# Optimization experiments

Hardware: AMD Instinct MI355X
Metric: run time of the kernel (lower is better)

The kernel has to match this reference:

```python
import jax, jax.numpy as jnp
import numpy as np
import math

B, S, IN_DIM = 2048, 60, 211
D, H, L, DFF, NC = 192, 6, 3, 768, 35
DK = D // H


def make_pe(seq_len, d_model):
    pos = np.arange(seq_len)[:, None].astype(np.float32)
    div = np.exp(np.arange(0, d_model, 2).astype(np.float32) * (-math.log(10000.0) / d_model))
    pe = np.zeros((seq_len, d_model), dtype=np.float32)
    pe[:, 0::2] = np.sin(pos * div)
    pe[:, 1::2] = np.cos(pos * div)
    return jnp.asarray(pe)


def setup_inputs() -> dict:
    key = jax.random.key(0)
    ks = jax.random.split(key, 24)
    r = lambda k, shape, fan: jax.random.normal(k, shape, jnp.float32) * (1.0 / np.sqrt(fan))
    inp = {
        'x': jax.random.normal(ks[0], (B, S, IN_DIM), jnp.float32),
        'W_in': r(ks[1], (IN_DIM, D), IN_DIM), 'b_in': jnp.zeros((D,), jnp.float32),
        'pe': make_pe(S, D),
        'Wq': r(ks[2], (L, D, D), D), 'bq': jnp.zeros((L, D), jnp.float32),
        'Wk': r(ks[3], (L, D, D), D), 'bk': jnp.zeros((L, D), jnp.float32),
        'Wv': r(ks[4], (L, D, D), D), 'bv': jnp.zeros((L, D), jnp.float32),
        'Wo': r(ks[5], (L, D, D), D), 'bo': jnp.zeros((L, D), jnp.float32),
        'W1': r(ks[6], (L, D, DFF), D), 'b1': jnp.zeros((L, DFF), jnp.float32),
        'W2': r(ks[7], (L, DFF, D), DFF), 'b2': jnp.zeros((L, D), jnp.float32),
        'g1': jnp.ones((L, D), jnp.float32), 'be1': jnp.zeros((L, D), jnp.float32),
        'g2': jnp.ones((L, D), jnp.float32), 'be2': jnp.zeros((L, D), jnp.float32),
        'Wc1': r(ks[8], (D, D // 2), D), 'bc1': jnp.zeros((D // 2,), jnp.float32),
        'Wc2': r(ks[9], (D // 2, NC), D // 2), 'bc2': jnp.zeros((NC,), jnp.float32),
    }
    return inp


def layer_norm(x, g, b, eps=1e-5):
    mu = jnp.mean(x, axis=-1, keepdims=True)
    var = jnp.mean((x - mu) ** 2, axis=-1, keepdims=True)
    return (x - mu) * jax.lax.rsqrt(var + eps) * g + b


def mha(x, Wq, bq, Wk, bk, Wv, bv, Wo, bo):
    Bs, Ss, _ = x.shape
    q = (x @ Wq + bq).reshape(Bs, Ss, H, DK)
    k = (x @ Wk + bk).reshape(Bs, Ss, H, DK)
    v = (x @ Wv + bv).reshape(Bs, Ss, H, DK)
    scores = jnp.einsum('bqhd,bkhd->bhqk', q, k) / jnp.sqrt(jnp.float32(DK))
    attn = jax.nn.softmax(scores, axis=-1)
    ctx = jnp.einsum('bhqk,bkhd->bqhd', attn, v).reshape(Bs, Ss, D)
    return ctx @ Wo + bo


def encoder_layer(x, Wq, bq, Wk, bk, Wv, bv, Wo, bo, W1, b1, W2, b2, g1, be1, g2, be2):
    attn_out = mha(x, Wq, bq, Wk, bk, Wv, bv, Wo, bo)
    x = layer_norm(x + attn_out, g1, be1)
    ff = jax.nn.gelu(x @ W1 + b1, approximate=False) @ W2 + b2
    return layer_norm(x + ff, g2, be2)


def reference(x, W_in, b_in, pe, Wq, bq, Wk, bk, Wv, bv, Wo, bo,
              W1, b1, W2, b2, g1, be1, g2, be2, Wc1, bc1, Wc2, bc2):
    h = x @ W_in + b_in + pe  # [B,S,D]
    for l in range(L):
        h = encoder_layer(h, Wq[l], bq[l], Wk[l], bk[l], Wv[l], bv[l], Wo[l], bo[l],
                          W1[l], b1[l], W2[l], b2[l], g1[l], be1[l], g2[l], be2[l])
    hidden = jax.nn.gelu(h @ Wc1 + bc1, approximate=False)
    return hidden @ Wc2 + bc2  # [B,S,NC]
```

## Files before the change

### kernel.cpp

```cpp
#include <hip/hip_runtime.h>
#include <cmath>

#define B_   2048
#define S_   60
#define NTOK (B_*S_)
#define IND_ 211
#define D_   192
#define H_   6
#define DK_  32
#define L_   3
#define DFF_ 768
#define NC_  35
#define DH_  96

typedef unsigned short us_t;
typedef us_t us8 __attribute__((ext_vector_type(8)));
typedef us_t us4 __attribute__((ext_vector_type(4)));
typedef short sh8 __attribute__((ext_vector_type(8)));
typedef float f4 __attribute__((ext_vector_type(4)));

#define MFMA(a, b, cc) __builtin_amdgcn_mfma_f32_16x16x32_bf16((a), (b), (cc), 0, 0, 0)
#define ZACC(A, M, N) \
    for (int _i = 0; _i < (M); ++_i) \
        for (int _j = 0; _j < (N); ++_j) { \
            A[_i][_j][0] = 0.f; A[_i][_j][1] = 0.f; A[_i][_j][2] = 0.f; A[_i][_j][3] = 0.f; }
#define ZACC1(A, N) \
    for (int _j = 0; _j < (N); ++_j) { \
        A[_j][0] = 0.f; A[_j][1] = 0.f; A[_j][2] = 0.f; A[_j][3] = 0.f; }

__device__ __forceinline__ float bf2f(us_t u) {
    union { unsigned int i; float f; } v; v.i = ((unsigned int)u) << 16; return v.f;
}
__device__ __forceinline__ us_t f2bf(float f) {
    union { float f; unsigned int i; } v; v.f = f;
    unsigned int r = v.i + 0x7fffu + ((v.i >> 16) & 1u);
    return (us_t)(r >> 16);
}
__device__ __forceinline__ float gelu_f(float v) {
    float u = v * (0.7978845608f + 0.0356774081f * v * v);
    float e = __expf(2.f * u);
    float t = 1.f - 2.f / (e + 1.f);
    return 0.5f * v * (1.f + t);
}
__device__ __forceinline__ void gld16(const us_t* g, us_t* s) {
    __builtin_amdgcn_global_load_lds(
        (const __attribute__((address_space(1))) unsigned int*)(g),
        (__attribute__((address_space(3))) unsigned int*)(s), 16, 0, 0);
}

__global__ void prep_misc(const float* __restrict__ W_in, const float* __restrict__ Wc1,
                          us_t* __restrict__ Wint, us_t* __restrict__ Wc1t)
{
    int e = blockIdx.x * 256 + threadIdx.x;
    const int n1 = 192 * 224, n2 = 96 * 192;
    if (e < n1) {
        int n = e / 224, kp = e % 224;
        Wint[e] = (kp < IND_) ? f2bf(W_in[(size_t)kp * D_ + n]) : (us_t)0;
    } else if (e < n1 + n2) {
        int r = e - n1;
        int n = r / 192, kp = r % 192;
        Wc1t[r] = f2bf(Wc1[(size_t)kp * DH_ + n]);
    }
}

__global__ void prep_qkvw(const float* __restrict__ Wq, const float* __restrict__ Wk,
                          const float* __restrict__ Wv, const float* __restrict__ Wo,
                          us_t* __restrict__ WI)
{
    int e = blockIdx.x * 256 + threadIdx.x;
    if (e >= L_ * 12 * 13824) return;
    int l = e / (12 * 13824), r = e % (12 * 13824);
    int t = r / 13824, q = r % 13824;
    int rw = q / 72, kk = q % 72;
    us_t v = 0;
    if (kk < 64) {
        int mat = (t < 9) ? (t / 3) : 3;
        int pc  = (t < 9) ? (t % 3) : (t - 9);
        const float* W = (mat == 0) ? Wq : (mat == 1) ? Wk : (mat == 2) ? Wv : Wo;
        v = f2bf(W[(size_t)l * 36864 + (size_t)(pc * 64 + kk) * D_ + rw]);
    }
    WI[e] = v;
}

__global__ void prep_ff(const float* __restrict__ W1, const float* __restrict__ W2,
                        us_t* __restrict__ W1T, us_t* __restrict__ W2T)
{
    int e = blockIdx.x * 256 + threadIdx.x;
    if (e >= L_ * 12 * 13824) return;
    int l = e / (12 * 13824), r = e % (12 * 13824);
    int tile = r / 13824, q = r % 13824;
    int col = q / 72, kk = q % 72;
    int cb = tile / 3, pc = tile % 3;
    us_t v1 = 0, v2 = 0;
    if (kk < 64) {
        v1 = f2bf(W1[((size_t)l * D_ + pc * 64 + kk) * DFF_ + cb * D_ + col]);
        v2 = f2bf(W2[((size_t)l * DFF_ + cb * D_ + pc * 64 + kk) * D_ + col]);
    }
    W1T[e] = v1; W2T[e] = v2;
}

__global__ __launch_bounds__(256) void inp_mfma(
    const float* __restrict__ x, const us_t* __restrict__ Wint,
    const float* __restrict__ b_in, const float* __restrict__ pe,
    us_t* __restrict__ h)
{
    __shared__ __align__(16) char smem[29696 + 27648];
    us_t* Xs = (us_t*)smem;
    us_t* Ws = (us_t*)(smem + 29696);
    const int tid = threadIdx.x;
    const int lane = tid & 63, wid = tid >> 6;
    const int g = lane >> 4, c = lane & 15;
    const int wr = wid >> 1, wc = wid & 1;
    const int row0 = blockIdx.x * 64;

    for (int e = tid; e < 64 * 224; e += 256) {
        int tok = e / 224, kp = e % 224;
        float v = (kp < IND_) ? x[(size_t)(row0 + tok) * IND_ + kp] : 0.f;
        Xs[tok * 232 + kp] = f2bf(v);
    }

    f4 acc[2][6];
    ZACC(acc, 2, 6);
    for (int pc = 0; pc < 4; ++pc) {
        __syncthreads();
        const int nk = (pc < 3) ? 64 : 32;
        const int per = nk / 8;
        for (int e = tid; e < 192 * per; e += 256) {
            int rw = e / per, v = e % per;
            *(us8*)&Ws[rw * 72 + v * 8] =
                *(const us8*)&Wint[(size_t)rw * 224 + pc * 64 + v * 8];
        }
        __syncthreads();
        for (int kk = 0; kk < nk / 32; ++kk) {
            const int ka = pc * 64 + kk * 32 + g * 8;
            const int kw = kk * 32 + g * 8;
            sh8 a0 = *(const sh8*)&Xs[(32 * wr + c) * 232 + ka];
            sh8 a1 = *(const sh8*)&Xs[(32 * wr + 16 + c) * 232 + ka];
            #pragma unroll
            for (int ni = 0; ni < 6; ++ni) {
                sh8 bf = *(const sh8*)&Ws[(96 * wc + 16 * ni + c) * 72 + kw];
                acc[0][ni] = MFMA(a0, bf, acc[0][ni]);
                acc[1][ni] = MFMA(a1, bf, acc[1][ni]);
            }
        }
    }
    #pragma unroll
    for (int ni = 0; ni < 6; ++ni) {
        const int col = 96 * wc + 16 * ni + c;
        const float bv = b_in[col];
        #pragma unroll
        for (int mi = 0; mi < 2; ++mi)
            #pragma unroll
            for (int r = 0; r < 4; ++r) {
                int tokg = row0 + 32 * wr + 16 * mi + 4 * g + r;
                int s = tokg % S_;
                float val = acc[mi][ni][r] + bv + pe[(size_t)s * D_ + col];
                h[(size_t)tokg * D_ + col] = f2bf(val);
            }
    }
}

__global__ __launch_bounds__(1024) void qkv_attn_wo(
    us_t* __restrict__ h, const us_t* __restrict__ WI,
    const float* __restrict__ bq, const float* __restrict__ bk,
    const float* __restrict__ bv, const float* __restrict__ bo,
    const float* __restrict__ g1, const float* __restrict__ be1)
{
    __shared__ __align__(16) char smem[159744];
    us_t* Xs  = (us_t*)smem;
    us_t* Qs  = (us_t*)(smem + 25600);
    us_t* Ks  = (us_t*)(smem + 51200);
    us_t* Vt  = (us_t*)(smem + 76800);
    us_t* Wsb = (us_t*)(smem + 104448);
    us_t* P6  = (us_t*)(smem + 104448);
    us_t* Cx  = (us_t*)(smem + 25600);
    float* eL = (float*)(smem + 51200);

    const int tid = threadIdx.x;
    const int lane = tid & 63, wid = tid >> 6;
    const int g = lane >> 4, c = lane & 15;
    const int wr = wid >> 2, wc = wid & 3;
    us_t* hb = h + (size_t)blockIdx.x * (S_ * D_);

    auto stageI = [&](int t) {
        const us_t* src = WI + (size_t)t * 13824;
        us_t* dst = Wsb + (size_t)(t & 1) * 13824;
        for (int i = wid; i < 27; i += 16)
            gld16(src + i * 512 + lane * 8, dst + i * 512);
    };

    for (int e = tid; e < 1536; e += 1024) {
        int tok = e / 24, v = e % 24;
        us8 u = {0, 0, 0, 0, 0, 0, 0, 0};
        if (tok < S_) u = *(const us8*)&hb[(size_t)tok * D_ + v * 8];
        *(us8*)&Xs[tok * 200 + v * 8] = u;
    }
    stageI(0);
    __syncthreads();

    for (int m = 0; m < 3; ++m) {
        const float* bb = (m == 0) ? bq : (m == 1) ? bk : bv;
        f4 acc[3];
        ZACC1(acc, 3);
        for (int pc = 0; pc < 3; ++pc) {
            const int t = m * 3 + pc;
            if (t < 8) stageI(t + 1);
            const us_t* W = Wsb + (size_t)(t & 1) * 13824;
            #pragma unroll
            for (int kk = 0; kk < 2; ++kk) {
                const int ka = pc * 64 + kk * 32 + g * 8;
                const int kw = kk * 32 + g * 8;
                sh8 a0 = *(const sh8*)&Xs[(16 * wr + c) * 200 + ka];
                #pragma unroll
                for (int ni = 0; ni < 3; ++ni) {
                    sh8 bf = *(const sh8*)&W[(48 * wc + 16 * ni + c) * 72 + kw];
                    acc[ni] = MFMA(a0, bf, acc[ni]);
                }
            }
            __syncthreads();
        }
        #pragma unroll
        for (int ni = 0; ni < 3; ++ni) {
            const int col = 48 * wc + 16 * ni + c;
            const float bval = bb[col];
            #pragma unroll
            for (int r = 0; r < 4; ++r) {
                int tok = 16 * wr + 4 * g + r;
                us_t o = f2bf(acc[ni][r] + bval);
                if (m == 0)      Qs[tok * 200 + col] = o;
                else if (m == 1) Ks[tok * 200 + col] = o;
                else             Vt[col * 72 + tok] = o;
            }
        }
    }
    __syncthreads();

    for (int r2 = 0; r2 < 2; ++r2) {
        if (wid < 12) {
            const int hh = 3 * r2 + (wid >> 2);
            const int hgrp = wid & 3;
            us_t* Pb = P6 + (size_t)hh * 4608;
            f4 sc[4];
            ZACC1(sc, 4);
            const int ka = 32 * hh + g * 8;
            sh8 aq = *(const sh8*)&Qs[(16 * hgrp + c) * 200 + ka];
            #pragma unroll
            for (int ni = 0; ni < 4; ++ni) {
                sh8 bk8 = *(const sh8*)&Ks[(16 * ni + c) * 200 + ka];
                sc[ni] = MFMA(aq, bk8, sc[ni]);
            }
            #pragma unroll
            for (int r = 0; r < 4; ++r) {
                float mx = -1e30f;
                #pragma unroll
                for (int ni = 0; ni < 4; ++ni) {
                    float v = sc[ni][r] * 0.17677669529663687f;
                    if (16 * ni + c >= S_) v = -1e30f;
                    sc[ni][r] = v;
                    mx = fmaxf(mx, v);
                }
                mx = fmaxf(mx, __shfl_xor(mx, 1));
                mx = fmaxf(mx, __shfl_xor(mx, 2));
                mx = fmaxf(mx, __shfl_xor(mx, 4));
                mx = fmaxf(mx, __shfl_xor(mx, 8));
                float sum = 0.f;
                #pragma unroll
                for (int ni = 0; ni < 4; ++ni) {
                    float e = __expf(sc[ni][r] - mx);
                    sc[ni][r] = e; sum += e;
                }
                sum += __shfl_xor(sum, 1);
                sum += __shfl_xor(sum, 2);
                sum += __shfl_xor(sum, 4);
                sum += __shfl_xor(sum, 8);
                const float inv = 1.f / sum;
                #pragma unroll
                for (int ni = 0; ni < 4; ++ni)
                    Pb[(16 * hgrp + 4 * g + r) * 72 + 16 * ni + c] = f2bf(sc[ni][r] * inv);
            }
        }
    }
    __syncthreads();

    for (int r2 = 0; r2 < 2; ++r2) {
        if (wid < 12) {
            const int hh = 3 * r2 + (wid >> 2);
            const int hgrp = wid & 3;
            const us_t* Pb = P6 + (size_t)hh * 4608;
            f4 ov[2];
            ZACC1(ov, 2);
            #pragma unroll
            for (int kk = 0; kk < 2; ++kk) {
                sh8 ap = *(const sh8*)&Pb[(16 * hgrp + c) * 72 + kk * 32 + g * 8];
                #pragma unroll
                for (int n2 = 0; n2 < 2; ++n2) {
                    sh8 bv8 = *(const sh8*)&Vt[(32 * hh + 16 * n2 + c) * 72 + kk * 32 + g * 8];
                    ov[n2] = MFMA(ap, bv8, ov[n2]);
                }
            }
            #pragma unroll
            for (int n2 = 0; n2 < 2; ++n2)
                #pragma unroll
                for (int r = 0; r < 4; ++r)
                    Cx[(16 * hgrp + 4 * g + r) * 200 + 32 * hh + 16 * n2 + c] = f2bf(ov[n2][r]);
        }
    }
    __syncthreads();

    stageI(9);
    __syncthreads();
    f4 aw[3];
    ZACC1(aw, 3);
    for (int pc = 0; pc < 3; ++pc) {
        const int t = 9 + pc;
        if (pc < 2) stageI(t + 1);
        const us_t* W = Wsb + (size_t)(t & 1) * 13824;
        #pragma unroll
        for (int kk = 0; kk < 2; ++kk) {
            const int ka = pc * 64 + kk * 32 + g * 8;
            const int kw = kk * 32 + g * 8;
            sh8 a0 = *(const sh8*)&Cx[(16 * wr + c) * 200 + ka];
            #pragma unroll
            for (int ni = 0; ni < 3; ++ni) {
                sh8 bf = *(const sh8*)&W[(48 * wc + 16 * ni + c) * 72 + kw];
                aw[ni] = MFMA(a0, bf, aw[ni]);
            }
        }
        __syncthreads();
    }
    #pragma unroll
    for (int ni = 0; ni < 3; ++ni) {
        const int col = 48 * wc + 16 * ni + c;
        const float bov = bo[col];
        #pragma unroll
        for (int r = 0; r < 4; ++r) {
            int tok = 16 * wr + 4 * g + r;
            eL[tok * 200 + col] = aw[ni][r] + bov + bf2f(Xs[tok * 200 + col]);
        }
    }
    __syncthreads();
    {
        const int tl = tid >> 4, t16 = tid & 15;
        float vals[12], sum = 0.f, ssq = 0.f;
        #pragma unroll
        for (int jv = 0; jv < 3; ++jv) {
            float4 v4 = *(const float4*)&eL[tl * 200 + t16 * 12 + jv * 4];
            vals[jv*4+0] = v4.x; vals[jv*4+1] = v4.y; vals[jv*4+2] = v4.z; vals[jv*4+3] = v4.w;
            sum += v4.x + v4.y + v4.z + v4.w;
            ssq += v4.x*v4.x + v4.y*v4.y + v4.z*v4.z + v4.w*v4.w;
        }
        sum += __shfl_xor(sum, 1); sum += __shfl_xor(sum, 2);
        sum += __shfl_xor(sum, 4); sum += __shfl_xor(sum, 8);
        ssq += __shfl_xor(ssq, 1); ssq += __shfl_xor(ssq, 2);
        ssq += __shfl_xor(ssq, 4); ssq += __shfl_xor(ssq, 8);
        const float mean = sum * (1.f / D_);
        const float var  = ssq * (1.f / D_) - mean * mean;
        const float rstd = rsqrtf(var + 1e-5f);
        if (tl < S_) {
            #pragma unroll
            for (int jv = 0; jv < 3; ++jv) {
                us4 o4;
                #pragma unroll
                for (int j = 0; j < 4; ++j) {
                    int col = t16 * 12 + jv * 4 + j;
                    o4[j] = f2bf((vals[jv*4+j] - mean) * rstd * g1[col] + be1[col]);
                }
                *(us4*)&hb[(size_t)tl * D_ + t16 * 12 + jv * 4] = o4;
            }
        }
    }
}

__global__ __launch_bounds__(1024) void ff_mfma(
    us_t* __restrict__ hio,
    const us_t* __restrict__ W1T, const float* __restrict__ b1,
    const us_t* __restrict__ W2T, const float* __restrict__ b2,
    const float* __restrict__ gamma, const float* __restrict__ beta)
{
    __shared__ __align__(16) char smem[157696];
    us_t* Xs  = (us_t*)smem;
    us_t* Ts  = (us_t*)(smem + 51200);
    us_t* Wsb = (us_t*)(smem + 102400);
    float* eL = (float*)(smem + 51200);

    const int tid = threadIdx.x;
    const int lane = tid & 63, wid = tid >> 6;
    const int g = lane >> 4, c = lane & 15;
    const int wr = wid >> 2, wc = wid & 3;
    const int row0 = blockIdx.x * 128;

    auto stageW = [&](int t) {
        const int cb2 = t / 6, ph = (t % 6) / 3, pc2 = t % 3;
        const us_t* src = (ph ? W2T : W1T) + (size_t)(cb2 * 3 + pc2) * 13824;
        us_t* dst = Wsb + (size_t)(t & 1) * 13824;
        for (int i = wid; i < 27; i += 16)
            gld16(src + i * 512 + lane * 8, dst + i * 512);
    };

    for (int e = tid; e < 3072; e += 1024) {
        int tok = e / 24, v = e % 24;
        *(us8*)&Xs[tok * 200 + v * 8] = *(const us8*)&hio[(size_t)(row0 + tok) * D_ + v * 8];
    }
    stageW(0);
    __syncthreads();

    f4 acc2[2][3];
    ZACC(acc2, 2, 3);
    for (int cb = 0; cb < 4; ++cb) {
        f4 acc1[2][3];
        ZACC(acc1, 2, 3);
        #pragma unroll
        for (int pc = 0; pc < 3; ++pc) {
            const int t = cb * 6 + pc;
            if (t < 23) stageW(t + 1);
            const us_t* W = Wsb + (size_t)(t & 1) * 13824;
            #pragma unroll
            for (int kk = 0; kk < 2; ++kk) {
                const int ka = pc * 64 + kk * 32 + g * 8;
                const int kw = kk * 32 + g * 8;
                sh8 a0 = *(const sh8*)&Xs[(32 * wr + c) * 200 + ka];
                sh8 a1 = *(const sh8*)&Xs[(32 * wr + 16 + c) * 200 + ka];
                #pragma unroll
                for (int ni = 0; ni < 3; ++ni) {
                    sh8 bf = *(const sh8*)&W[(48 * wc + 16 * ni + c) * 72 + kw];
                    acc1[0][ni] = MFMA(a0, bf, acc1[0][ni]);
                    acc1[1][ni] = MFMA(a1, bf, acc1[1][ni]);
                }
            }
            if (pc == 2) {
                #pragma unroll
                for (int ni = 0; ni < 3; ++ni) {
                    const int col = 48 * wc + 16 * ni + c;
                    const float b1v = b1[cb * 192 + col];
                    #pragma unroll
                    for (int mi = 0; mi < 2; ++mi)
                        #pragma unroll
                        for (int r = 0; r < 4; ++r) {
                            int tok = 32 * wr + 16 * mi + 4 * g + r;
                            Ts[tok * 200 + col] = f2bf(gelu_f(acc1[mi][ni][r] + b1v));
                        }
                }
            }
            __syncthreads();
        }
        #pragma unroll
        for (int pc = 0; pc < 3; ++pc) {
            const int t = cb * 6 + 3 + pc;
            if (t < 23) stageW(t + 1);
            const us_t* W = Wsb + (size_t)(t & 1) * 13824;
            #pragma unroll
            for (int kk = 0; kk < 2; ++kk) {
                const int ka = pc * 64 + kk * 32 + g * 8;
                const int kw = kk * 32 + g * 8;
                sh8 a0 = *(const sh8*)&Ts[(32 * wr + c) * 200 + ka];
                sh8 a1 = *(const sh8*)&Ts[(32 * wr + 16 + c) * 200 + ka];
                #pragma unroll
                for (int ni = 0; ni < 3; ++ni) {
                    sh8 bf = *(const sh8*)&W[(48 * wc + 16 * ni + c) * 72 + kw];
                    acc2[0][ni] = MFMA(a0, bf, acc2[0][ni]);
                    acc2[1][ni] = MFMA(a1, bf, acc2[1][ni]);
                }
            }
            __syncthreads();
        }
    }

    for (int p = 0; p < 2; ++p) {
        if (p) __syncthreads();
        if ((wr >> 1) == p) {
            #pragma unroll
            for (int ni = 0; ni < 3; ++ni) {
                const int col = 48 * wc + 16 * ni + c;
                const float b2v = b2[col];
                #pragma unroll
                for (int mi = 0; mi < 2; ++mi)
                    #pragma unroll
                    for (int r = 0; r < 4; ++r) {
                        int tok = 32 * wr + 16 * mi + 4 * g + r;
                        eL[(tok - 64 * p) * 200 + col] =
                            acc2[mi][ni][r] + b2v + bf2f(Xs[tok * 200 + col]);
                    }
            }
        }
        __syncthreads();
        {
            const int tl = tid >> 4, t16 = tid & 15;
            float vals[12], sum = 0.f, ssq = 0.f;
            #pragma unroll
            for (int jv = 0; jv < 3; ++jv) {
                float4 v4 = *(const float4*)&eL[tl * 200 + t16 * 12 + jv * 4];
                vals[jv*4+0] = v4.x; vals[jv*4+1] = v4.y;
                vals[jv*4+2] = v4.z; vals[jv*4+3] = v4.w;
                sum += v4.x + v4.y + v4.z + v4.w;
                ssq += v4.x*v4.x + v4.y*v4.y + v4.z*v4.z + v4.w*v4.w;
            }
            sum += __shfl_xor(sum, 1); sum += __shfl_xor(sum, 2);
            sum += __shfl_xor(sum, 4); sum += __shfl_xor(sum, 8);
            ssq += __shfl_xor(ssq, 1); ssq += __shfl_xor(ssq, 2);
            ssq += __shfl_xor(ssq, 4); ssq += __shfl_xor(ssq, 8);
            const float mean = sum * (1.f / D_);
            const float var  = ssq * (1.f / D_) - mean * mean;
            const float rstd = rsqrtf(var + 1e-5f);
            #pragma unroll
            for (int jv = 0; jv < 3; ++jv) {
                us4 o4;
                #pragma unroll
                for (int j = 0; j < 4; ++j) {
                    int col = t16 * 12 + jv * 4 + j;
                    o4[j] = f2bf((vals[jv*4+j] - mean) * rstd * gamma[col] + beta[col]);
                }
                *(us4*)&hio[(size_t)(row0 + 64 * p + tl) * D_ + t16 * 12 + jv * 4] = o4;
            }
        }
    }
}

__global__ __launch_bounds__(256) void clf12(
    const us_t* __restrict__ h, const us_t* __restrict__ Wc1t,
    const float* __restrict__ bc1, const float* __restrict__ Wc2,
    const float* __restrict__ bc2, float* __restrict__ out)
{
    __shared__ __align__(16) char smem[25600 + 13824 + 13312];
    us_t* Xs = (us_t*)smem;
    us_t* Ws = (us_t*)(smem + 25600);
    us_t* Hs = (us_t*)(smem + 25600 + 13824);
    __shared__ float Wl[DH_ * NC_];
    __shared__ float bl[NC_];
    const int tid = threadIdx.x;
    const int lane = tid & 63, wid = tid >> 6;
    const int g = lane >> 4, c = lane & 15;
    const int wr = wid >> 1, wc = wid & 1;
    const int row0 = blockIdx.x * 64;

    for (int e = tid; e < 1536; e += 256) {
        int tok = e / 24, v = e % 24;
        *(us8*)&Xs[tok * 200 + v * 8] = *(const us8*)&h[(size_t)(row0 + tok) * D_ + v * 8];
    }
    for (int e = tid; e < DH_ * NC_; e += 256) Wl[e] = Wc2[e];
    if (tid < NC_) bl[tid] = bc2[tid];

    f4 acc[2][3];
    ZACC(acc, 2, 3);
    for (int pc = 0; pc < 3; ++pc) {
        __syncthreads();
        for (int e = tid; e < 768; e += 256) {
            int rw = e >> 3, v = e & 7;
            *(us8*)&Ws[rw * 72 + v * 8] =
                *(const us8*)&Wc1t[(size_t)rw * 192 + pc * 64 + v * 8];
        }
        __syncthreads();
        #pragma unroll
        for (int kk = 0; kk < 2; ++kk) {
            const int ka = pc * 64 + kk * 32 + g * 8;
            const int kw = kk * 32 + g * 8;
            sh8 a0 = *(const sh8*)&Xs[(32 * wr + c) * 200 + ka];
            sh8 a1 = *(const sh8*)&Xs[(32 * wr + 16 + c) * 200 + ka];
            #pragma unroll
            for (int ni = 0; ni < 3; ++ni) {
                sh8 bf = *(const sh8*)&Ws[(48 * wc + 16 * ni + c) * 72 + kw];
                acc[0][ni] = MFMA(a0, bf, acc[0][ni]);
                acc[1][ni] = MFMA(a1, bf, acc[1][ni]);
            }
        }
    }
    #pragma unroll
    for (int ni = 0; ni < 3; ++ni) {
        const int col = 48 * wc + 16 * ni + c;
        const float bv = bc1[col];
        #pragma unroll
        for (int mi = 0; mi < 2; ++mi)
            #pragma unroll
            for (int r = 0; r < 4; ++r) {
                int tok = 32 * wr + 16 * mi + 4 * g + r;
                Hs[tok * 104 + col] = f2bf(gelu_f(acc[mi][ni][r] + bv));
            }
    }
    __syncthreads();
    for (int e = tid; e < 64 * NC_; e += 256) {
        const int tok = e / NC_, col = e % NC_;
        float a = bl[col];
        #pragma unroll 8
        for (int kk = 0; kk < DH_; ++kk)
            a = fmaf(bf2f(Hs[tok * 104 + kk]), Wl[kk * NC_ + col], a);
        out[(size_t)(row0 + tok) * NC_ + col] = a;
    }
}

extern "C" void kernel_launch(void* const* d_in, const int* in_sizes, int n_in,
                              void* d_out, int out_size, void* d_ws, size_t ws_size,
                              hipStream_t stream)
{
    const float* x    = (const float*)d_in[0];
    const float* W_in = (const float*)d_in[1];
    const float* b_in = (const float*)d_in[2];
    const float* pe   = (const float*)d_in[3];
    const float* Wq   = (const float*)d_in[4];
    const float* bq   = (const float*)d_in[5];
    const float* Wk   = (const float*)d_in[6];
    const float* bk   = (const float*)d_in[7];
    const float* Wv   = (const float*)d_in[8];
    const float* bv   = (const float*)d_in[9];
    const float* Wo   = (const float*)d_in[10];
    const float* bo   = (const float*)d_in[11];
    const float* W1   = (const float*)d_in[12];
    const float* b1   = (const float*)d_in[13];
    const float* W2   = (const float*)d_in[14];
    const float* b2   = (const float*)d_in[15];
    const float* g1   = (const float*)d_in[16];
    const float* be1  = (const float*)d_in[17];
    const float* g2   = (const float*)d_in[18];
    const float* be2  = (const float*)d_in[19];
    const float* Wc1  = (const float*)d_in[20];
    const float* bc1  = (const float*)d_in[21];
    const float* Wc2  = (const float*)d_in[22];
    const float* bc2  = (const float*)d_in[23];
    float* outp = (float*)d_out;

    us_t* h    = (us_t*)d_ws;
    us_t* Wint = h + (size_t)NTOK * D_;
    us_t* WIq  = Wint + 192 * 224;
    us_t* W1T  = WIq + (size_t)L_ * 12 * 13824;
    us_t* W2T  = W1T + (size_t)L_ * 12 * 13824;
    us_t* Wc1t = W2T + (size_t)L_ * 12 * 13824;

    prep_misc<<<(192 * 224 + 96 * 192 + 255) / 256, 256, 0, stream>>>(W_in, Wc1, Wint, Wc1t);
    prep_qkvw<<<(L_ * 12 * 13824 + 255) / 256, 256, 0, stream>>>(Wq, Wk, Wv, Wo, WIq);
    prep_ff<<<(L_ * 12 * 13824 + 255) / 256, 256, 0, stream>>>(W1, W2, W1T, W2T);

    inp_mfma<<<NTOK / 64, 256, 0, stream>>>(x, Wint, b_in, pe, h);

    for (int l = 0; l < L_; ++l) {
        qkv_attn_wo<<<B_, 1024, 0, stream>>>(
            h, WIq + (size_t)l * 12 * 13824,
            bq + l * D_, bk + l * D_, bv + l * D_, bo + l * D_,
            g1 + l * D_, be1 + l * D_);
        ff_mfma<<<NTOK / 128, 1024, 0, stream>>>(
            h, W1T + (size_t)l * 12 * 13824, b1 + l * DFF_,
            W2T + (size_t)l * 12 * 13824, b2 + l * D_,
            g2 + l * D_, be2 + l * D_);
    }

    clf12<<<NTOK / 64, 256, 0, stream>>>(h, Wc1t, bc1, Wc2, bc2, outp);
}
```

Before: 1.109 ms.

## Read FF weight fragments directly from global memory instead of LDS staging

The FFN kernel no longer double-buffers W1/W2 tiles through shared memory. Each wave now loads its B-operand fragments straight from global (L2-cached) memory in a compact 64-wide layout, and most per-tile barriers are removed. This cuts LDS use from about 154KB to 100KB and drops the staging traffic and synchronisation. In exchange, every wave issues redundant global loads with higher latency and no prefetch overlap.

```diff
diff --git a/kernel.cpp b/kernel.cpp
--- a/kernel.cpp
+++ b/kernel.cpp
@@ -86,17 +86,13 @@
                         us_t* __restrict__ W1T, us_t* __restrict__ W2T)
 {
     int e = blockIdx.x * 256 + threadIdx.x;
-    if (e >= L_ * 12 * 13824) return;
-    int l = e / (12 * 13824), r = e % (12 * 13824);
-    int tile = r / 13824, q = r % 13824;
-    int col = q / 72, kk = q % 72;
+    if (e >= L_ * 12 * 12288) return;
+    int l = e / (12 * 12288), r = e % (12 * 12288);
+    int tile = r / 12288, q = r % 12288;
+    int col = q >> 6, kk = q & 63;
     int cb = tile / 3, pc = tile % 3;
-    us_t v1 = 0, v2 = 0;
-    if (kk < 64) {
-        v1 = f2bf(W1[((size_t)l * D_ + pc * 64 + kk) * DFF_ + cb * D_ + col]);
-        v2 = f2bf(W2[((size_t)l * DFF_ + cb * D_ + pc * 64 + kk) * D_ + col]);
-    }
-    W1T[e] = v1; W2T[e] = v2;
+    W1T[e] = f2bf(W1[((size_t)l * D_ + pc * 64 + kk) * DFF_ + cb * D_ + col]);
+    W2T[e] = f2bf(W2[((size_t)l * DFF_ + cb * D_ + pc * 64 + kk) * D_ + col]);
 }
 
 __global__ __launch_bounds__(256) void inp_mfma(
@@ -377,10 +373,9 @@
     const us_t* __restrict__ W2T, const float* __restrict__ b2,
     const float* __restrict__ gamma, const float* __restrict__ beta)
 {
-    __shared__ __align__(16) char smem[157696];
+    __shared__ __align__(16) char smem[102400];
     us_t* Xs  = (us_t*)smem;
     us_t* Ts  = (us_t*)(smem + 51200);
-    us_t* Wsb = (us_t*)(smem + 102400);
     float* eL = (float*)(smem + 51200);
 
     const int tid = threadIdx.x;
@@ -389,19 +384,10 @@
     const int wr = wid >> 2, wc = wid & 3;
     const int row0 = blockIdx.x * 128;
 
-    auto stageW = [&](int t) {
-        const int cb2 = t / 6, ph = (t % 6) / 3, pc2 = t % 3;
-        const us_t* src = (ph ? W2T : W1T) + (size_t)(cb2 * 3 + pc2) * 13824;
-        us_t* dst = Wsb + (size_t)(t & 1) * 13824;
-        for (int i = wid; i < 27; i += 16)
-            gld16(src + i * 512 + lane * 8, dst + i * 512);
-    };
-
     for (int e = tid; e < 3072; e += 1024) {
         int tok = e / 24, v = e % 24;
         *(us8*)&Xs[tok * 200 + v * 8] = *(const us8*)&hio[(size_t)(row0 + tok) * D_ + v * 8];
     }
-    stageW(0);
     __syncthreads();
 
     f4 acc2[2][3];
@@ -411,9 +397,7 @@
         ZACC(acc1, 2, 3);
         #pragma unroll
         for (int pc = 0; pc < 3; ++pc) {
-            const int t = cb * 6 + pc;
-            if (t < 23) stageW(t + 1);
-            const us_t* W = Wsb + (size_t)(t & 1) * 13824;
+            const us_t* W = W1T + (size_t)(cb * 3 + pc) * 12288;
             #pragma unroll
             for (int kk = 0; kk < 2; ++kk) {
                 const int ka = pc * 64 + kk * 32 + g * 8;
@@ -422,32 +406,28 @@
                 sh8 a1 = *(const sh8*)&Xs[(32 * wr + 16 + c) * 200 + ka];
                 #pragma unroll
                 for (int ni = 0; ni < 3; ++ni) {
-                    sh8 bf = *(const sh8*)&W[(48 * wc + 16 * ni + c) * 72 + kw];
+                    sh8 bf = *(const sh8*)&W[(size_t)(48 * wc + 16 * ni + c) * 64 + kw];
                     acc1[0][ni] = MFMA(a0, bf, acc1[0][ni]);
                     acc1[1][ni] = MFMA(a1, bf, acc1[1][ni]);
                 }
             }
-            if (pc == 2) {
-                #pragma unroll
-                for (int ni = 0; ni < 3; ++ni) {
-                    const int col = 48 * wc + 16 * ni + c;
-                    const float b1v = b1[cb * 192 + col];
-                    #pragma unroll
-                    for (int mi = 0; mi < 2; ++mi)
-                        #pragma unroll
-                        for (int r = 0; r < 4; ++r) {
-                            int tok = 32 * wr + 16 * mi + 4 * g + r;
-                            Ts[tok * 200 + col] = f2bf(gelu_f(acc1[mi][ni][r] + b1v));
-                        }
-                }
-            }
-            __syncthreads();
-        }
+        }
+        #pragma unroll
+        for (int ni = 0; ni < 3; ++ni) {
+            const int col = 48 * wc + 16 * ni + c;
+            const float b1v = b1[cb * 192 + col];
+            #pragma unroll
+            for (int mi = 0; mi < 2; ++mi)
+                #pragma unroll
+                for (int r = 0; r < 4; ++r) {
+                    int tok = 32 * wr + 16 * mi + 4 * g + r;
+                    Ts[tok * 200 + col] = f2bf(gelu_f(acc1[mi][ni][r] + b1v));
+                }
+        }
+        __syncthreads();
         #pragma unroll
         for (int pc = 0; pc < 3; ++pc) {
-            const int t = cb * 6 + 3 + pc;
-            if (t < 23) stageW(t + 1);
-            const us_t* W = Wsb + (size_t)(t & 1) * 13824;
+            const us_t* W = W2T + (size_t)(cb * 3 + pc) * 12288;
             #pragma unroll
             for (int kk = 0; kk < 2; ++kk) {
                 const int ka = pc * 64 + kk * 32 + g * 8;
@@ -456,13 +436,13 @@
                 sh8 a1 = *(const sh8*)&Ts[(32 * wr + 16 + c) * 200 + ka];
                 #pragma unroll
                 for (int ni = 0; ni < 3; ++ni) {
-                    sh8 bf = *(const sh8*)&W[(48 * wc + 16 * ni + c) * 72 + kw];
+                    sh8 bf = *(const sh8*)&W[(size_t)(48 * wc + 16 * ni + c) * 64 + kw];
                     acc2[0][ni] = MFMA(a0, bf, acc2[0][ni]);
                     acc2[1][ni] = MFMA(a1, bf, acc2[1][ni]);
                 }
             }
-            __syncthreads();
-        }
+        }
+        __syncthreads();
     }
 
     for (int p = 0; p < 2; ++p) {
@@ -620,12 +600,12 @@
     us_t* Wint = h + (size_t)NTOK * D_;
     us_t* WIq  = Wint + 192 * 224;
     us_t* W1T  = WIq + (size_t)L_ * 12 * 13824;
-    us_t* W2T  = W1T + (size_t)L_ * 12 * 13824;
-    us_t* Wc1t = W2T + (size_t)L_ * 12 * 13824;
+    us_t* W2T  = W1T + (size_t)L_ * 12 * 12288;
+    us_t* Wc1t = W2T + (size_t)L_ * 12 * 12288;
 
     prep_misc<<<(192 * 224 + 96 * 192 + 255) / 256, 256, 0, stream>>>(W_in, Wc1, Wint, Wc1t);
     prep_qkvw<<<(L_ * 12 * 13824 + 255) / 256, 256, 0, stream>>>(Wq, Wk, Wv, Wo, WIq);
-    prep_ff<<<(L_ * 12 * 13824 + 255) / 256, 256, 0, stream>>>(W1, W2, W1T, W2T);
+    prep_ff<<<(L_ * 12 * 12288 + 255) / 256, 256, 0, stream>>>(W1, W2, W1T, W2T);
 
     inp_mfma<<<NTOK / 64, 256, 0, stream>>>(x, Wint, b_in, pe, h);
 
@@ -635,8 +615,8 @@
             bq + l * D_, bk + l * D_, bv + l * D_, bo + l * D_,
             g1 + l * D_, be1 + l * D_);
         ff_mfma<<<NTOK / 128, 1024, 0, stream>>>(
-            h, W1T + (size_t)l * 12 * 13824, b1 + l * DFF_,
-            W2T + (size_t)l * 12 * 13824, b2 + l * D_,
+            h, W1T + (size_t)l * 12 * 12288, b1 + l * DFF_,
+            W2T + (size_t)l * 12 * 12288, b2 + l * D_,
             g2 + l * D_, be2 + l * D_);
     }
 
```

Measured after the change: 1.636 ms. 1.48x slower.
